# Kernel tuning notes

Hardware: AMD Instinct MI355X
Metric: run time of the kernel (lower is better)

The kernel has to match this reference:

```python
import jax, jax.numpy as jnp
import numpy as np

N, E, T, H, D_IN, D_OUT = 50000, 320000, 4, 4, 128, 128
NEG_SLOPE = 0.2
LN_EPS = 1e-5


def setup_inputs() -> dict:
    key = jax.random.key(0)
    ks = jax.random.split(key, 10)
    x = jax.random.normal(ks[0], (N, D_IN), jnp.float32)
    edge_index = jax.random.randint(ks[1], (2, E), 0, N, jnp.int32)
    edge_attr = jax.random.randint(ks[2], (E,), 0, T, jnp.int32)
    W_gat = jax.random.normal(ks[3], (T, D_IN, H * D_OUT), jnp.float32) / np.sqrt(D_IN)
    a_src = jax.random.normal(ks[4], (T, H, D_OUT), jnp.float32) / np.sqrt(D_OUT)
    a_dst = jax.random.normal(ks[5], (T, H, D_OUT), jnp.float32) / np.sqrt(D_OUT)
    b_gat = jnp.zeros((T, D_OUT), jnp.float32)
    edge_type_weights = jnp.ones((T,), jnp.float32) / T
    W_fuse = jax.random.normal(ks[6], (T * D_OUT, D_OUT), jnp.float32) / np.sqrt(T * D_OUT)
    b_fuse = jnp.zeros((D_OUT,), jnp.float32)
    ln_gamma = jnp.ones((D_OUT,), jnp.float32)
    ln_beta = jnp.zeros((D_OUT,), jnp.float32)
    return {"x": x, "edge_index": edge_index, "edge_attr": edge_attr,
            "W_gat": W_gat, "a_src": a_src, "a_dst": a_dst, "b_gat": b_gat,
            "edge_type_weights": edge_type_weights, "W_fuse": W_fuse,
            "b_fuse": b_fuse, "ln_gamma": ln_gamma, "ln_beta": ln_beta}


def _gat_one_type(x, src_all, dst_all, mask_all, W, a_s, a_d, b):
    # x: [N, D_in]; src_all/dst_all: [E+N] (type-mask + self-loops on all nodes)
    n = x.shape[0]
    h = (x @ W).reshape(n, H, D_OUT)                      # [N, H, D]
    alpha_s = jnp.sum(h * a_s, axis=-1)                   # [N, H]
    alpha_d = jnp.sum(h * a_d, axis=-1)                   # [N, H]
    logit = jax.nn.leaky_relu(alpha_s[src_all] + alpha_d[dst_all], NEG_SLOPE)  # [Ea, H]
    neg_inf = jnp.float32(-1e30)
    logit = jnp.where(mask_all[:, None], logit, neg_inf)
    m = jax.ops.segment_max(logit, dst_all, num_segments=n)   # [N, H] (self-loops ensure finite)
    ex = jnp.exp(logit - m[dst_all])
    ex = jnp.where(mask_all[:, None], ex, 0.0)
    denom = jax.ops.segment_sum(ex, dst_all, num_segments=n)  # [N, H]
    alpha = ex / denom[dst_all]                                # [Ea, H]
    msg = alpha[:, :, None] * h[src_all]                       # [Ea, H, D]
    out = jax.ops.segment_sum(msg, dst_all, num_segments=n)   # [N, H, D]
    return out.mean(axis=1) + b                                # concat=False -> head mean


def reference(x, edge_index, edge_attr, W_gat, a_src, a_dst, b_gat,
              edge_type_weights, W_fuse, b_fuse, ln_gamma, ln_beta):
    n = x.shape[0]
    self_idx = jnp.arange(n, dtype=edge_index.dtype)
    src_all = jnp.concatenate([edge_index[0], self_idx])
    dst_all = jnp.concatenate([edge_index[1], self_idx])
    outs = []
    for t in range(T):
        mask_all = jnp.concatenate([edge_attr == t, jnp.ones((n,), bool)])
        outs.append(_gat_one_type(x, src_all, dst_all, mask_all,
                                  W_gat[t], a_src[t], a_dst[t], b_gat[t]))
    w = jax.nn.softmax(edge_type_weights)
    x_cat = jnp.concatenate([outs[t] * w[t] for t in range(T)], axis=1)  # [N, T*D]
    y = x_cat @ W_fuse + b_fuse
    mu = jnp.mean(y, axis=-1, keepdims=True)
    var = jnp.var(y, axis=-1, keepdims=True)
    y = (y - mu) / jnp.sqrt(var + LN_EPS) * ln_gamma + ln_beta
    return jax.nn.relu(y)
```

## Files before the change

kernel.cpp:

```cpp
#include <hip/hip_runtime.h>
#include <hip/hip_bf16.h>

#define TT 4
#define HH 4
#define DD 128
#define KAGG 2048

typedef __attribute__((ext_vector_type(8))) short short8;
typedef __attribute__((ext_vector_type(4))) float f32x4;
typedef __attribute__((ext_vector_type(4))) unsigned int uint4v;

__device__ __forceinline__ float lrelu(float z) { return z > 0.f ? z : 0.2f * z; }
__device__ __forceinline__ float bf2f(unsigned short u) {
  union { unsigned int i; float f; } v; v.i = ((unsigned int)u) << 16; return v.f;
}
__device__ __forceinline__ unsigned short f2b(float f) {
  union { float f; unsigned int i; } u; u.f = f;
  unsigned int r = u.i + 0x7fff + ((u.i >> 16) & 1);
  return (unsigned short)(r >> 16);
}
__device__ __forceinline__ void unpack8v(uint4v u, float* hv) {
  hv[0] = bf2f((unsigned short)(u.x & 0xffff));
  hv[1] = bf2f((unsigned short)(u.x >> 16));
  hv[2] = bf2f((unsigned short)(u.y & 0xffff));
  hv[3] = bf2f((unsigned short)(u.y >> 16));
  hv[4] = bf2f((unsigned short)(u.z & 0xffff));
  hv[5] = bf2f((unsigned short)(u.z >> 16));
  hv[6] = bf2f((unsigned short)(u.w & 0xffff));
  hv[7] = bf2f((unsigned short)(u.w >> 16));
}

__global__ __launch_bounds__(256) void prologue_kernel(
    const float* __restrict__ x, unsigned short* __restrict__ xb, int total4,
    const float* __restrict__ Wg, const float* __restrict__ a_s,
    const float* __restrict__ a_d, const float* __restrict__ W_fuse,
    const float* __restrict__ b_gat, const float* __restrict__ etw,
    const float* __restrict__ b_fuse, unsigned short* __restrict__ Pall,
    float* __restrict__ cbias, const int* __restrict__ dst,
    const int* __restrict__ attr, int* __restrict__ deg, int E, int N) {
  int bid = blockIdx.x;
  const int nconv = (total4 + 255) >> 8;
  if (bid < nconv) {
    int i = bid * 256 + threadIdx.x;
    if (i < total4) {
      float4 v = ((const float4*)x)[i];
      ushort4 o;
      o.x = f2b(v.x); o.y = f2b(v.y); o.z = f2b(v.z); o.w = f2b(v.w);
      ((ushort4*)xb)[i] = o;
    }
    return;
  }
  bid -= nconv;
  if (bid < 17) {
    float e0 = etw[0], e1 = etw[1], e2 = etw[2], e3 = etw[3];
    float mx = fmaxf(fmaxf(e0, e1), fmaxf(e2, e3));
    float w0 = __expf(e0 - mx), w1 = __expf(e1 - mx), w2 = __expf(e2 - mx),
          w3 = __expf(e3 - mx);
    float inv = 1.f / (w0 + w1 + w2 + w3);
    float wts[4] = {w0 * inv, w1 * inv, w2 * inv, w3 * inv};
    if (bid < 16) {
      int idx = bid * 256 + threadIdx.x;
      int c = idx >> 7, k = idx & 127;
      int t = c >> 3, jj = c & 7, head = jj & 3;
      const float* av = ((jj < 4) ? a_s : a_d) + (t * 4 + head) * 128;
      const float* wr = Wg + (size_t)t * 65536 + k * 512 + head * 128;
      float s = 0.f;
      for (int m = 0; m < 128; ++m) s += wr[m] * av[m];
      Pall[c * 128 + k] = f2b(s);
    } else {
      int j = threadIdx.x;
      if (j < 128) {
        float s = b_fuse[j];
        for (int t = 0; t < 4; ++t) {
          float st = 0.f;
          for (int m = 0; m < 128; ++m)
            st += b_gat[t * 128 + m] * W_fuse[(size_t)(t * 128 + m) * 128 + j];
          s += wts[t] * st;
        }
        cbias[j] = s;
      }
    }
    return;
  }
  bid -= 17;
  int e = bid * 256 + threadIdx.x;
  if (e < E) atomicAdd(&deg[attr[e] * N + dst[e]], 1);
}

__global__ __launch_bounds__(256) void gprep_kernel(
    const float* __restrict__ Wg, const float* __restrict__ W_fuse,
    const float* __restrict__ etw, unsigned short* __restrict__ Gfrag) {
  __shared__ float Bs[128][128];
  int t = blockIdx.x >> 6;
  int kr0 = (blockIdx.x & 63) * 8;
  const float* wf = W_fuse + (size_t)t * 16384;
#pragma unroll
  for (int i = 0; i < 64; ++i)
    ((float*)Bs)[i * 256 + threadIdx.x] = wf[i * 256 + threadIdx.x];

  float e0 = etw[0], e1 = etw[1], e2 = etw[2], e3 = etw[3];
  float mx = fmaxf(fmaxf(e0, e1), fmaxf(e2, e3));
  float w0 = __expf(e0 - mx), w1 = __expf(e1 - mx), w2 = __expf(e2 - mx),
        w3 = __expf(e3 - mx);
  float inv = 1.f / (w0 + w1 + w2 + w3);
  float wt = ((t == 0) ? w0 : (t == 1) ? w1 : (t == 2) ? w2 : w3) * inv * 0.25f;
  __syncthreads();

  int rr = threadIdx.x >> 7;
  int j  = threadIdx.x & 127;
#pragma unroll
  for (int r2 = 0; r2 < 4; ++r2) {
    int kr = kr0 + r2 * 2 + rr;
    int head = kr >> 7, k = kr & 127;
    const float* wr = Wg + (size_t)t * 65536 + k * 512 + head * 128;
    float s = 0.f;
    for (int m = 0; m < 128; ++m) s += wr[m] * Bs[m][j];
    s *= wt;
    int K = t * 512 + kr;
    int kt = K >> 7, kk = (K >> 5) & 3, n = j >> 4;
    int f = (kt * 4 + kk) * 8 + n;
    int lg = (K >> 3) & 3, lr = j & 15, j8 = K & 7;
    Gfrag[(size_t)f * 512 + (lg * 16 + lr) * 8 + j8] = f2b(s);
  }
}

__global__ __launch_bounds__(1024) void scanfused_kernel(
    const int* __restrict__ deg, int* __restrict__ rowptr,
    int* __restrict__ cursor, int* __restrict__ gcur, int M) {
  __shared__ int sh[1024];
  __shared__ int base;
  int i = blockIdx.x * 1024 + threadIdx.x;
  int v = (i < M) ? deg[i] : 0;
  sh[threadIdx.x] = v;
  __syncthreads();
  for (int off = 1; off < 1024; off <<= 1) {
    int xx = (threadIdx.x >= off) ? sh[threadIdx.x - off] : 0;
    __syncthreads();
    sh[threadIdx.x] += xx;
    __syncthreads();
  }
  if (threadIdx.x == 1023) base = atomicAdd(gcur, sh[1023]);
  __syncthreads();
  if (i < M) {
    int r = base + sh[threadIdx.x] - v;
    rowptr[i] = r;
    cursor[i] = r;
  }
}

__global__ __launch_bounds__(256) void scatter_alpha_kernel(
    const int* __restrict__ src, const int* __restrict__ dst,
    const int* __restrict__ attr, int* __restrict__ cursor,
    int* __restrict__ slist, const unsigned short* __restrict__ xb,
    const unsigned short* __restrict__ Pall, float* __restrict__ as_,
    float* __restrict__ ad_, int E, int N) {
  __shared__ uint4 ldsv[2048];
  int bid = blockIdx.x;
  const int nsc = (E + 255) >> 8;
  if (bid < nsc) {
    int e = bid * 256 + threadIdx.x;
    if (e < E) {
      int p = atomicAdd(&cursor[attr[e] * N + dst[e]], 1);
      slist[p] = src[e];
    }
    return;
  }
  bid -= nsc;
  unsigned char* lds = (unsigned char*)ldsv;
  const int n0 = bid * 128;
  const int tid = threadIdx.x, lane = tid & 63, wid = tid >> 6;
  const int lr = lane & 15, lg = lane >> 4;
#pragma unroll
  for (int i = 0; i < 8; ++i) {
    int chunk = tid + i * 256;
    int row = chunk >> 4, k16 = chunk & 15;
    int gr = n0 + row;
    uint4 v = make_uint4(0, 0, 0, 0);
    if (gr < N) v = *(const uint4*)(xb + (size_t)gr * DD + k16 * 8);
    *(uint4*)(lds + ((row * 256 + k16 * 16) ^ ((row & 7) << 4))) = v;
  }
  __syncthreads();
  f32x4 acc[2][2] = {};
#pragma unroll
  for (int kk = 0; kk < 4; ++kk) {
    short8 a[2], b[2];
#pragma unroll
    for (int m = 0; m < 2; ++m) {
      int row = wid * 32 + m * 16 + lr;
      a[m] = *(const short8*)(lds + ((row * 256 + kk * 64 + (lg << 4)) ^ ((row & 7) << 4)));
    }
#pragma unroll
    for (int n = 0; n < 2; ++n) {
      int c = n * 16 + lr;
      b[n] = *(const short8*)(Pall + c * DD + kk * 32 + lg * 8);
    }
#pragma unroll
    for (int m = 0; m < 2; ++m)
#pragma unroll
      for (int n = 0; n < 2; ++n)
        acc[m][n] = __builtin_amdgcn_mfma_f32_16x16x32_bf16(a[m], b[n], acc[m][n], 0, 0, 0);
  }
#pragma unroll
  for (int m = 0; m < 2; ++m)
#pragma unroll
    for (int n = 0; n < 2; ++n) {
      int c = n * 16 + lr;
      int t = c >> 3, jj = c & 7, head = jj & 3;
      float* dstp = (jj & 4) ? ad_ : as_;
#pragma unroll
      for (int r = 0; r < 4; ++r) {
        int gr = n0 + wid * 32 + m * 16 + lg * 4 + r;
        if (gr < N) dstp[((size_t)t * N + gr) * 4 + head] = acc[m][n][r];
      }
    }
}

__global__ __launch_bounds__(256) void gather_kernel(
    const int* __restrict__ slist, const int* __restrict__ rowptr,
    const int* __restrict__ deg, const float* __restrict__ as_,
    const float* __restrict__ ad_, const unsigned short* __restrict__ xb,
    unsigned short* __restrict__ AGG, int N) {
  int t = blockIdx.y;
  int lane = threadIdx.x & 63;
  int u = lane >> 4, c16 = lane & 15;
  int d = blockIdx.x * 16 + (threadIdx.x >> 6) * 4 + u;
  if (d >= N) return;
  size_t tn = (size_t)t * N;
  int dofs = c16 * 8;
  unsigned short* outp = AGG + (size_t)d * KAGG + t * 512 + dofs;

  int base = rowptr[tn + d], dg = deg[tn + d];
  uint4v uself = *(const uint4v*)(xb + (size_t)d * DD + dofs);
  if (dg == 0) {
#pragma unroll
    for (int h = 0; h < 4; ++h) *(uint4v*)(outp + h * DD) = uself;
    return;
  }

  float4 ad4 = *(const float4*)(ad_ + (tn + d) * 4);
  float4 av = *(const float4*)(as_ + (tn + d) * 4);
  float q[4], den[4], hv[8], acc[4][8];
  q[0] = __expf(lrelu(av.x + ad4.x));
  q[1] = __expf(lrelu(av.y + ad4.y));
  q[2] = __expf(lrelu(av.z + ad4.z));
  q[3] = __expf(lrelu(av.w + ad4.w));
  unpack8v(uself, hv);
#pragma unroll
  for (int h = 0; h < 4; ++h) {
    den[h] = q[h];
#pragma unroll
    for (int j = 0; j < 8; ++j) acc[h][j] = q[h] * hv[j];
  }

  int i = 0;
  for (; i + 3 < dg; i += 4) {
    int s0 = slist[base + i], s1 = slist[base + i + 1];
    int s2 = slist[base + i + 2], s3 = slist[base + i + 3];
    float4 a0 = *(const float4*)(as_ + (tn + s0) * 4);
    float4 a1 = *(const float4*)(as_ + (tn + s1) * 4);
    float4 a2 = *(const float4*)(as_ + (tn + s2) * 4);
    float4 a3 = *(const float4*)(as_ + (tn + s3) * 4);
    uint4v u0 = *(const uint4v*)(xb + (size_t)s0 * DD + dofs);
    uint4v u1 = *(const uint4v*)(xb + (size_t)s1 * DD + dofs);
    uint4v u2 = *(const uint4v*)(xb + (size_t)s2 * DD + dofs);
    uint4v u3 = *(const uint4v*)(xb + (size_t)s3 * DD + dofs);
    float qq[4][4];
    qq[0][0] = __expf(lrelu(a0.x + ad4.x));
    qq[0][1] = __expf(lrelu(a0.y + ad4.y));
    qq[0][2] = __expf(lrelu(a0.z + ad4.z));
    qq[0][3] = __expf(lrelu(a0.w + ad4.w));
    qq[1][0] = __expf(lrelu(a1.x + ad4.x));
    qq[1][1] = __expf(lrelu(a1.y + ad4.y));
    qq[1][2] = __expf(lrelu(a1.z + ad4.z));
    qq[1][3] = __expf(lrelu(a1.w + ad4.w));
    qq[2][0] = __expf(lrelu(a2.x + ad4.x));
    qq[2][1] = __expf(lrelu(a2.y + ad4.y));
    qq[2][2] = __expf(lrelu(a2.z + ad4.z));
    qq[2][3] = __expf(lrelu(a2.w + ad4.w));
    qq[3][0] = __expf(lrelu(a3.x + ad4.x));
    qq[3][1] = __expf(lrelu(a3.y + ad4.y));
    qq[3][2] = __expf(lrelu(a3.z + ad4.z));
    qq[3][3] = __expf(lrelu(a3.w + ad4.w));
#pragma unroll
    for (int h = 0; h < 4; ++h)
      den[h] += qq[0][h] + qq[1][h] + qq[2][h] + qq[3][h];
    unpack8v(u0, hv);
#pragma unroll
    for (int h = 0; h < 4; ++h)
#pragma unroll
      for (int j = 0; j < 8; ++j) acc[h][j] += qq[0][h] * hv[j];
    unpack8v(u1, hv);
#pragma unroll
    for (int h = 0; h < 4; ++h)
#pragma unroll
      for (int j = 0; j < 8; ++j) acc[h][j] += qq[1][h] * hv[j];
    unpack8v(u2, hv);
#pragma unroll
    for (int h = 0; h < 4; ++h)
#pragma unroll
      for (int j = 0; j < 8; ++j) acc[h][j] += qq[2][h] * hv[j];
    unpack8v(u3, hv);
#pragma unroll
    for (int h = 0; h < 4; ++h)
#pragma unroll
      for (int j = 0; j < 8; ++j) acc[h][j] += qq[3][h] * hv[j];
  }
  for (; i < dg; ++i) {
    int s = slist[base + i];
    float4 a = *(const float4*)(as_ + (tn + s) * 4);
    uint4v ue = *(const uint4v*)(xb + (size_t)s * DD + dofs);
    float qe[4];
    qe[0] = __expf(lrelu(a.x + ad4.x));
    qe[1] = __expf(lrelu(a.y + ad4.y));
    qe[2] = __expf(lrelu(a.z + ad4.z));
    qe[3] = __expf(lrelu(a.w + ad4.w));
#pragma unroll
    for (int h = 0; h < 4; ++h) den[h] += qe[h];
    unpack8v(ue, hv);
#pragma unroll
    for (int h = 0; h < 4; ++h)
#pragma unroll
      for (int j = 0; j < 8; ++j) acc[h][j] += qe[h] * hv[j];
  }

#pragma unroll
  for (int h = 0; h < 4; ++h) {
    float r = 1.f / den[h];
    uint4v o;
    o.x = (unsigned)f2b(acc[h][0] * r) | ((unsigned)f2b(acc[h][1] * r) << 16);
    o.y = (unsigned)f2b(acc[h][2] * r) | ((unsigned)f2b(acc[h][3] * r) << 16);
    o.z = (unsigned)f2b(acc[h][4] * r) | ((unsigned)f2b(acc[h][5] * r) << 16);
    o.w = (unsigned)f2b(acc[h][6] * r) | ((unsigned)f2b(acc[h][7] * r) << 16);
    *(uint4v*)(outp + h * DD) = o;
  }
}

__global__ __launch_bounds__(256) void gemmln_kernel(
    const unsigned short* __restrict__ AGG, const unsigned short* __restrict__ Gfrag,
    const float* __restrict__ cbias, const float* __restrict__ gamma,
    const float* __restrict__ beta, float* __restrict__ out, int N) {
  __shared__ uint4 bbuf[2][1024];
  const int n0 = blockIdx.x * 64;
  const int tid = threadIdx.x, lane = tid & 63, wid = tid >> 6;
  const int lr = lane & 15, lg = lane >> 4;
  const int wrow = n0 + wid * 16;
  const int gr = wrow + lr;
  const bool ok = gr < N;
  const unsigned short* arow = AGG + (size_t)gr * KAGG;

  uint4 bn[4], an[2], ac[2];
#pragma unroll
  for (int i = 0; i < 4; ++i)
    bn[i] = *(const uint4*)(Gfrag + (size_t)(i * 256 + tid) * 8);
#pragma unroll
  for (int kkh = 0; kkh < 2; ++kkh) {
    an[kkh] = make_uint4(0, 0, 0, 0);
    if (ok) an[kkh] = *(const uint4*)(arow + kkh * 32 + lg * 8);
  }
#pragma unroll
  for (int i = 0; i < 4; ++i) bbuf[0][i * 256 + tid] = bn[i];
  ac[0] = an[0]; ac[1] = an[1];
  __syncthreads();

  f32x4 acc[8] = {};
  int cur = 0;
  for (int ht = 0; ht < 32; ++ht) {
    if (ht < 31) {
#pragma unroll
      for (int i = 0; i < 4; ++i)
        bn[i] = *(const uint4*)(Gfrag + (size_t)(ht + 1) * 8192 +
                                (size_t)(i * 256 + tid) * 8);
#pragma unroll
      for (int kkh = 0; kkh < 2; ++kkh) {
        an[kkh] = make_uint4(0, 0, 0, 0);
        if (ok) an[kkh] = *(const uint4*)(arow + (ht + 1) * 64 + kkh * 32 + lg * 8);
      }
    }
    const unsigned char* lds = (const unsigned char*)bbuf[cur];
#pragma unroll
    for (int kkh = 0; kkh < 2; ++kkh) {
      short8 a = *(const short8*)&ac[kkh];
#pragma unroll
      for (int n = 0; n < 8; ++n) {
        short8 b = *(const short8*)(lds + (kkh * 8 + n) * 1024 + lane * 16);
        acc[n] = __builtin_amdgcn_mfma_f32_16x16x32_bf16(a, b, acc[n], 0, 0, 0);
      }
    }
    if (ht < 31) {
#pragma unroll
      for (int i = 0; i < 4; ++i) bbuf[cur ^ 1][i * 256 + tid] = bn[i];
      ac[0] = an[0]; ac[1] = an[1];
      __syncthreads();
      cur ^= 1;
    }
  }

  float cb[8], gm[8], bt[8];
#pragma unroll
  for (int n = 0; n < 8; ++n) {
    cb[n] = cbias[n * 16 + lr];
    gm[n] = gamma[n * 16 + lr];
    bt[n] = beta[n * 16 + lr];
  }
#pragma unroll
  for (int rr = 0; rr < 4; ++rr) {
    float y[8];
    float s = 0.f, ss = 0.f;
#pragma unroll
    for (int n = 0; n < 8; ++n) {
      y[n] = acc[n][rr] + cb[n];
      s += y[n];
      ss += y[n] * y[n];
    }
#pragma unroll
    for (int mask = 1; mask <= 8; mask <<= 1) {
      s += __shfl_xor(s, mask);
      ss += __shfl_xor(ss, mask);
    }
    float mean = s * (1.f / 128.f);
    float var = ss * (1.f / 128.f) - mean * mean;
    float rstd = rsqrtf(var + 1e-5f);
    int orow = wrow + lg * 4 + rr;
    if (orow < N) {
#pragma unroll
      for (int n = 0; n < 8; ++n) {
        float v = (y[n] - mean) * rstd * gm[n] + bt[n];
        out[(size_t)orow * DD + n * 16 + lr] = fmaxf(0.f, v);
      }
    }
  }
}

extern "C" void kernel_launch(void* const* d_in, const int* in_sizes, int n_in,
                              void* d_out, int out_size, void* d_ws, size_t ws_size,
                              hipStream_t stream) {
  const float* x      = (const float*)d_in[0];
  const int*   ei     = (const int*)d_in[1];
  const int*   attr   = (const int*)d_in[2];
  const float* Wg     = (const float*)d_in[3];
  const float* a_src  = (const float*)d_in[4];
  const float* a_dst  = (const float*)d_in[5];
  const float* b_gat  = (const float*)d_in[6];
  const float* etw    = (const float*)d_in[7];
  const float* W_fuse = (const float*)d_in[8];
  const float* b_fuse = (const float*)d_in[9];
  const float* gamma  = (const float*)d_in[10];
  const float* beta   = (const float*)d_in[11];

  const int N = in_sizes[0] / DD;
  const int E = in_sizes[2];
  const int* src = ei;
  const int* dst = ei + E;
  const int M = TT * N;

  char* ws = (char*)d_ws;
  size_t off = 0;
  auto alloc = [&](size_t bytes) {
    void* p = ws + off;
    off += (bytes + 255) & ~(size_t)255;
    return p;
  };
  unsigned short* AGG   = (unsigned short*)alloc((size_t)N * KAGG * 2);
  unsigned short* xb    = (unsigned short*)alloc((size_t)N * DD * 2);
  unsigned short* Gfrag = (unsigned short*)alloc((size_t)512 * 512 * 2);
  unsigned short* Pall  = (unsigned short*)alloc((size_t)32 * DD * 2);
  float* cbias          = (float*)alloc(128 * sizeof(float));
  float* as_            = (float*)alloc((size_t)TT * N * 4 * sizeof(float));
  float* ad_            = (float*)alloc((size_t)TT * N * 4 * sizeof(float));
  int* deg              = (int*)alloc((size_t)(M + 1) * sizeof(int));
  int* rowptr           = (int*)alloc((size_t)M * sizeof(int));
  int* cursor           = (int*)alloc((size_t)M * sizeof(int));
  int* slist            = (int*)alloc((size_t)E * sizeof(int));

  hipMemsetAsync(deg, 0, (size_t)(M + 1) * sizeof(int), stream);

  int total4x = N * DD / 4;
  int nconv = (total4x + 255) / 256;
  int nhist = (E + 255) / 256;
  prologue_kernel<<<nconv + 17 + nhist, 256, 0, stream>>>(
      x, xb, total4x, Wg, a_src, a_dst, W_fuse, b_gat, etw, b_fuse,
      Pall, cbias, dst, attr, deg, E, N);

  gprep_kernel<<<256, 256, 0, stream>>>(Wg, W_fuse, etw, Gfrag);

  scanfused_kernel<<<(M + 1023) / 1024, 1024, 0, stream>>>(deg, rowptr, cursor,
                                                           deg + M, M);

  int nalpha = (N + 127) / 128;
  scatter_alpha_kernel<<<nhist + nalpha, 256, 0, stream>>>(
      src, dst, attr, cursor, slist, xb, Pall, as_, ad_, E, N);

  dim3 ggrid((N + 15) / 16, TT);
  gather_kernel<<<ggrid, 256, 0, stream>>>(slist, rowptr, deg, as_, ad_, xb, AGG, N);

  gemmln_kernel<<<(N + 63) / 64, 256, 0, stream>>>(AGG, Gfrag, cbias, gamma, beta,
                                                   (float*)d_out, N);
}
```

Measured before the change: 210.5 us.

## Merge scan, weight prep and alpha GEMM into one launch; precompute edge exp weights

The scan, fused-weight preparation and per-node alpha projection now run as block-index-partitioned branches of a single stage2 kernel with a shared 64KB LDS buffer, which cuts launches. The edge scatter moves into its own kernel that also computes each edge's exp(leaky_relu) attention numerators and stores them in a new qlist beside the CSR source list. The gather kernel then streams these precomputed weights instead of gathering as_ per source and evaluating exp, and its unroll drops from 4 to 2. In exchange there is an extra 16 bytes per edge of writes and reads, a dependent kernel boundary between alpha computation and scatter, and scan blocks that now hold 64KB of LDS, which may lower occupancy.

```diff
diff --git a/kernel.cpp b/kernel.cpp
--- a/kernel.cpp
+++ b/kernel.cpp
@@ -87,86 +87,76 @@
   if (e < E) atomicAdd(&deg[attr[e] * N + dst[e]], 1);
 }
 
-__global__ __launch_bounds__(256) void gprep_kernel(
+__global__ __launch_bounds__(256) void stage2_kernel(
+    const int* __restrict__ deg, int* __restrict__ rowptr,
+    int* __restrict__ cursor, int* __restrict__ gcur, int M,
     const float* __restrict__ Wg, const float* __restrict__ W_fuse,
-    const float* __restrict__ etw, unsigned short* __restrict__ Gfrag) {
-  __shared__ float Bs[128][128];
-  int t = blockIdx.x >> 6;
-  int kr0 = (blockIdx.x & 63) * 8;
-  const float* wf = W_fuse + (size_t)t * 16384;
-#pragma unroll
-  for (int i = 0; i < 64; ++i)
-    ((float*)Bs)[i * 256 + threadIdx.x] = wf[i * 256 + threadIdx.x];
-
-  float e0 = etw[0], e1 = etw[1], e2 = etw[2], e3 = etw[3];
-  float mx = fmaxf(fmaxf(e0, e1), fmaxf(e2, e3));
-  float w0 = __expf(e0 - mx), w1 = __expf(e1 - mx), w2 = __expf(e2 - mx),
-        w3 = __expf(e3 - mx);
-  float inv = 1.f / (w0 + w1 + w2 + w3);
-  float wt = ((t == 0) ? w0 : (t == 1) ? w1 : (t == 2) ? w2 : w3) * inv * 0.25f;
-  __syncthreads();
-
-  int rr = threadIdx.x >> 7;
-  int j  = threadIdx.x & 127;
-#pragma unroll
-  for (int r2 = 0; r2 < 4; ++r2) {
-    int kr = kr0 + r2 * 2 + rr;
-    int head = kr >> 7, k = kr & 127;
-    const float* wr = Wg + (size_t)t * 65536 + k * 512 + head * 128;
-    float s = 0.f;
-    for (int m = 0; m < 128; ++m) s += wr[m] * Bs[m][j];
-    s *= wt;
-    int K = t * 512 + kr;
-    int kt = K >> 7, kk = (K >> 5) & 3, n = j >> 4;
-    int f = (kt * 4 + kk) * 8 + n;
-    int lg = (K >> 3) & 3, lr = j & 15, j8 = K & 7;
-    Gfrag[(size_t)f * 512 + (lg * 16 + lr) * 8 + j8] = f2b(s);
-  }
-}
-
-__global__ __launch_bounds__(1024) void scanfused_kernel(
-    const int* __restrict__ deg, int* __restrict__ rowptr,
-    int* __restrict__ cursor, int* __restrict__ gcur, int M) {
-  __shared__ int sh[1024];
-  __shared__ int base;
-  int i = blockIdx.x * 1024 + threadIdx.x;
-  int v = (i < M) ? deg[i] : 0;
-  sh[threadIdx.x] = v;
-  __syncthreads();
-  for (int off = 1; off < 1024; off <<= 1) {
-    int xx = (threadIdx.x >= off) ? sh[threadIdx.x - off] : 0;
+    const float* __restrict__ etw, unsigned short* __restrict__ Gfrag,
+    const unsigned short* __restrict__ xb, const unsigned short* __restrict__ Pall,
+    float* __restrict__ as_, float* __restrict__ ad_, int N) {
+  __shared__ __align__(16) unsigned char smem[65536 + 16];
+  int bid = blockIdx.x;
+  const int nscan = (M + 255) >> 8;
+  if (bid < nscan) {
+    int* sh = (int*)smem;
+    int* basep = (int*)(smem + 65536);
+    int i = bid * 256 + threadIdx.x;
+    int v = (i < M) ? deg[i] : 0;
+    sh[threadIdx.x] = v;
     __syncthreads();
-    sh[threadIdx.x] += xx;
+    for (int off = 1; off < 256; off <<= 1) {
+      int xx = (threadIdx.x >= off) ? sh[threadIdx.x - off] : 0;
+      __syncthreads();
+      sh[threadIdx.x] += xx;
+      __syncthreads();
+    }
+    if (threadIdx.x == 255) *basep = atomicAdd(gcur, sh[255]);
     __syncthreads();
-  }
-  if (threadIdx.x == 1023) base = atomicAdd(gcur, sh[1023]);
-  __syncthreads();
-  if (i < M) {
-    int r = base + sh[threadIdx.x] - v;
-    rowptr[i] = r;
-    cursor[i] = r;
-  }
-}
-
-__global__ __launch_bounds__(256) void scatter_alpha_kernel(
-    const int* __restrict__ src, const int* __restrict__ dst,
-    const int* __restrict__ attr, int* __restrict__ cursor,
-    int* __restrict__ slist, const unsigned short* __restrict__ xb,
-    const unsigned short* __restrict__ Pall, float* __restrict__ as_,
-    float* __restrict__ ad_, int E, int N) {
-  __shared__ uint4 ldsv[2048];
-  int bid = blockIdx.x;
-  const int nsc = (E + 255) >> 8;
-  if (bid < nsc) {
-    int e = bid * 256 + threadIdx.x;
-    if (e < E) {
-      int p = atomicAdd(&cursor[attr[e] * N + dst[e]], 1);
-      slist[p] = src[e];
+    if (i < M) {
+      int r = *basep + sh[threadIdx.x] - v;
+      rowptr[i] = r;
+      cursor[i] = r;
     }
     return;
   }
-  bid -= nsc;
-  unsigned char* lds = (unsigned char*)ldsv;
+  bid -= nscan;
+  if (bid < 256) {
+    float(*Bs)[128] = (float(*)[128])smem;
+    int t = bid >> 6;
+    int kr0 = (bid & 63) * 8;
+    const float* wf = W_fuse + (size_t)t * 16384;
+#pragma unroll
+    for (int i = 0; i < 64; ++i)
+      ((float*)Bs)[i * 256 + threadIdx.x] = wf[i * 256 + threadIdx.x];
+
+    float e0 = etw[0], e1 = etw[1], e2 = etw[2], e3 = etw[3];
+    float mx = fmaxf(fmaxf(e0, e1), fmaxf(e2, e3));
+    float w0 = __expf(e0 - mx), w1 = __expf(e1 - mx), w2 = __expf(e2 - mx),
+          w3 = __expf(e3 - mx);
+    float inv = 1.f / (w0 + w1 + w2 + w3);
+    float wt = ((t == 0) ? w0 : (t == 1) ? w1 : (t == 2) ? w2 : w3) * inv * 0.25f;
+    __syncthreads();
+
+    int rr = threadIdx.x >> 7;
+    int j = threadIdx.x & 127;
+#pragma unroll
+    for (int r2 = 0; r2 < 4; ++r2) {
+      int kr = kr0 + r2 * 2 + rr;
+      int head = kr >> 7, k = kr & 127;
+      const float* wr = Wg + (size_t)t * 65536 + k * 512 + head * 128;
+      float s = 0.f;
+      for (int m = 0; m < 128; ++m) s += wr[m] * Bs[m][j];
+      s *= wt;
+      int K = t * 512 + kr;
+      int kt = K >> 7, kk = (K >> 5) & 3, n = j >> 4;
+      int f = (kt * 4 + kk) * 8 + n;
+      int lg = (K >> 3) & 3, lr = j & 15, j8 = K & 7;
+      Gfrag[(size_t)f * 512 + (lg * 16 + lr) * 8 + j8] = f2b(s);
+    }
+    return;
+  }
+  bid -= 256;
+  unsigned char* lds = smem;
   const int n0 = bid * 128;
   const int tid = threadIdx.x, lane = tid & 63, wid = tid >> 6;
   const int lr = lane & 15, lg = lane >> 4;
@@ -215,11 +205,33 @@
     }
 }
 
+__global__ __launch_bounds__(256) void scatter_q_kernel(
+    const int* __restrict__ src, const int* __restrict__ dst,
+    const int* __restrict__ attr, int* __restrict__ cursor,
+    int* __restrict__ slist, float* __restrict__ qlist,
+    const float* __restrict__ as_, const float* __restrict__ ad_,
+    int E, int N) {
+  int e = blockIdx.x * 256 + threadIdx.x;
+  if (e >= E) return;
+  int t = attr[e], s = src[e], d = dst[e];
+  int p = atomicAdd(&cursor[(size_t)t * N + d], 1);
+  float4 a = *(const float4*)(as_ + ((size_t)t * N + s) * 4);
+  float4 b = *(const float4*)(ad_ + ((size_t)t * N + d) * 4);
+  float4 q;
+  q.x = __expf(lrelu(a.x + b.x));
+  q.y = __expf(lrelu(a.y + b.y));
+  q.z = __expf(lrelu(a.z + b.z));
+  q.w = __expf(lrelu(a.w + b.w));
+  slist[p] = s;
+  *(float4*)(qlist + (size_t)p * 4) = q;
+}
+
 __global__ __launch_bounds__(256) void gather_kernel(
-    const int* __restrict__ slist, const int* __restrict__ rowptr,
-    const int* __restrict__ deg, const float* __restrict__ as_,
-    const float* __restrict__ ad_, const unsigned short* __restrict__ xb,
-    unsigned short* __restrict__ AGG, int N) {
+    const int* __restrict__ slist, const float* __restrict__ qlist,
+    const int* __restrict__ rowptr, const int* __restrict__ deg,
+    const float* __restrict__ as_, const float* __restrict__ ad_,
+    const unsigned short* __restrict__ xb, unsigned short* __restrict__ AGG,
+    int N) {
   int t = blockIdx.y;
   int lane = threadIdx.x & 63;
   int u = lane >> 4, c16 = lane & 15;
@@ -239,81 +251,49 @@
 
   float4 ad4 = *(const float4*)(ad_ + (tn + d) * 4);
   float4 av = *(const float4*)(as_ + (tn + d) * 4);
-  float q[4], den[4], hv[8], acc[4][8];
-  q[0] = __expf(lrelu(av.x + ad4.x));
-  q[1] = __expf(lrelu(av.y + ad4.y));
-  q[2] = __expf(lrelu(av.z + ad4.z));
-  q[3] = __expf(lrelu(av.w + ad4.w));
-  unpack8v(uself, hv);
-#pragma unroll
-  for (int h = 0; h < 4; ++h) {
-    den[h] = q[h];
-#pragma unroll
-    for (int j = 0; j < 8; ++j) acc[h][j] = q[h] * hv[j];
+  float den[4], hv[8], acc[4][8];
+  {
+    float qs[4];
+    qs[0] = __expf(lrelu(av.x + ad4.x));
+    qs[1] = __expf(lrelu(av.y + ad4.y));
+    qs[2] = __expf(lrelu(av.z + ad4.z));
+    qs[3] = __expf(lrelu(av.w + ad4.w));
+    unpack8v(uself, hv);
+#pragma unroll
+    for (int h = 0; h < 4; ++h) {
+      den[h] = qs[h];
+#pragma unroll
+      for (int j = 0; j < 8; ++j) acc[h][j] = qs[h] * hv[j];
+    }
   }
 
   int i = 0;
-  for (; i + 3 < dg; i += 4) {
+  for (; i + 1 < dg; i += 2) {
     int s0 = slist[base + i], s1 = slist[base + i + 1];
-    int s2 = slist[base + i + 2], s3 = slist[base + i + 3];
-    float4 a0 = *(const float4*)(as_ + (tn + s0) * 4);
-    float4 a1 = *(const float4*)(as_ + (tn + s1) * 4);
-    float4 a2 = *(const float4*)(as_ + (tn + s2) * 4);
-    float4 a3 = *(const float4*)(as_ + (tn + s3) * 4);
+    float4 q0 = *(const float4*)(qlist + (size_t)(base + i) * 4);
+    float4 q1 = *(const float4*)(qlist + (size_t)(base + i + 1) * 4);
     uint4v u0 = *(const uint4v*)(xb + (size_t)s0 * DD + dofs);
     uint4v u1 = *(const uint4v*)(xb + (size_t)s1 * DD + dofs);
-    uint4v u2 = *(const uint4v*)(xb + (size_t)s2 * DD + dofs);
-    uint4v u3 = *(const uint4v*)(xb + (size_t)s3 * DD + dofs);
-    float qq[4][4];
-    qq[0][0] = __expf(lrelu(a0.x + ad4.x));
-    qq[0][1] = __expf(lrelu(a0.y + ad4.y));
-    qq[0][2] = __expf(lrelu(a0.z + ad4.z));
-    qq[0][3] = __expf(lrelu(a0.w + ad4.w));
-    qq[1][0] = __expf(lrelu(a1.x + ad4.x));
-    qq[1][1] = __expf(lrelu(a1.y + ad4.y));
-    qq[1][2] = __expf(lrelu(a1.z + ad4.z));
-    qq[1][3] = __expf(lrelu(a1.w + ad4.w));
-    qq[2][0] = __expf(lrelu(a2.x + ad4.x));
-    qq[2][1] = __expf(lrelu(a2.y + ad4.y));
-    qq[2][2] = __expf(lrelu(a2.z + ad4.z));
-    qq[2][3] = __expf(lrelu(a2.w + ad4.w));
-    qq[3][0] = __expf(lrelu(a3.x + ad4.x));
-    qq[3][1] = __expf(lrelu(a3.y + ad4.y));
-    qq[3][2] = __expf(lrelu(a3.z + ad4.z));
-    qq[3][3] = __expf(lrelu(a3.w + ad4.w));
+    float qa[4] = {q0.x, q0.y, q0.z, q0.w};
+    float qb[4] = {q1.x, q1.y, q1.z, q1.w};
+#pragma unroll
+    for (int h = 0; h < 4; ++h) den[h] += qa[h] + qb[h];
+    unpack8v(u0, hv);
 #pragma unroll
     for (int h = 0; h < 4; ++h)
-      den[h] += qq[0][h] + qq[1][h] + qq[2][h] + qq[3][h];
-    unpack8v(u0, hv);
+#pragma unroll
+      for (int j = 0; j < 8; ++j) acc[h][j] += qa[h] * hv[j];
+    unpack8v(u1, hv);
 #pragma unroll
     for (int h = 0; h < 4; ++h)
 #pragma unroll
-      for (int j = 0; j < 8; ++j) acc[h][j] += qq[0][h] * hv[j];
-    unpack8v(u1, hv);
-#pragma unroll
-    for (int h = 0; h < 4; ++h)
-#pragma unroll
-      for (int j = 0; j < 8; ++j) acc[h][j] += qq[1][h] * hv[j];
-    unpack8v(u2, hv);
-#pragma unroll
-    for (int h = 0; h < 4; ++h)
-#pragma unroll
-      for (int j = 0; j < 8; ++j) acc[h][j] += qq[2][h] * hv[j];
-    unpack8v(u3, hv);
-#pragma unroll
-    for (int h = 0; h < 4; ++h)
-#pragma unroll
-      for (int j = 0; j < 8; ++j) acc[h][j] += qq[3][h] * hv[j];
-  }
-  for (; i < dg; ++i) {
+      for (int j = 0; j < 8; ++j) acc[h][j] += qb[h] * hv[j];
+  }
+  if (i < dg) {
     int s = slist[base + i];
-    float4 a = *(const float4*)(as_ + (tn + s) * 4);
+    float4 q = *(const float4*)(qlist + (size_t)(base + i) * 4);
     uint4v ue = *(const uint4v*)(xb + (size_t)s * DD + dofs);
-    float qe[4];
-    qe[0] = __expf(lrelu(a.x + ad4.x));
-    qe[1] = __expf(lrelu(a.y + ad4.y));
-    qe[2] = __expf(lrelu(a.z + ad4.z));
-    qe[3] = __expf(lrelu(a.w + ad4.w));
+    float qe[4] = {q.x, q.y, q.z, q.w};
 #pragma unroll
     for (int h = 0; h < 4; ++h) den[h] += qe[h];
     unpack8v(ue, hv);
@@ -471,6 +451,7 @@
   int* rowptr           = (int*)alloc((size_t)M * sizeof(int));
   int* cursor           = (int*)alloc((size_t)M * sizeof(int));
   int* slist            = (int*)alloc((size_t)E * sizeof(int));
+  float* qlist          = (float*)alloc((size_t)E * 4 * sizeof(float));
 
   hipMemsetAsync(deg, 0, (size_t)(M + 1) * sizeof(int), stream);
 
@@ -481,17 +462,18 @@
       x, xb, total4x, Wg, a_src, a_dst, W_fuse, b_gat, etw, b_fuse,
       Pall, cbias, dst, attr, deg, E, N);
 
-  gprep_kernel<<<256, 256, 0, stream>>>(Wg, W_fuse, etw, Gfrag);
-
-  scanfused_kernel<<<(M + 1023) / 1024, 1024, 0, stream>>>(deg, rowptr, cursor,
-                                                           deg + M, M);
-
+  int nscan = (M + 255) / 256;
   int nalpha = (N + 127) / 128;
-  scatter_alpha_kernel<<<nhist + nalpha, 256, 0, stream>>>(
-      src, dst, attr, cursor, slist, xb, Pall, as_, ad_, E, N);
+  stage2_kernel<<<nscan + 256 + nalpha, 256, 0, stream>>>(
+      deg, rowptr, cursor, deg + M, M, Wg, W_fuse, etw, Gfrag,
+      xb, Pall, as_, ad_, N);
+
+  scatter_q_kernel<<<nhist, 256, 0, stream>>>(src, dst, attr, cursor, slist,
+                                              qlist, as_, ad_, E, N);
 
   dim3 ggrid((N + 15) / 16, TT);
-  gather_kernel<<<ggrid, 256, 0, stream>>>(slist, rowptr, deg, as_, ad_, xb, AGG, N);
+  gather_kernel<<<ggrid, 256, 0, stream>>>(slist, qlist, rowptr, deg, as_, ad_,
+                                           xb, AGG, N);
 
   gemmln_kernel<<<(N + 63) / 64, 256, 0, stream>>>(AGG, Gfrag, cbias, gamma, beta,
                                                    (float*)d_out, N);
```

Result: no change. 211.5 us (+0.5%).

## Split GEMM-LN output columns across 8 waves and shrink gather unroll

Applied to the files above, without the earlier changes.

The fused GEMM+LayerNorm kernel now runs 512 threads per block: two groups of four waves each compute half of the 128 output columns for the same 64 rows. Per-row LayerNorm partial sums are exchanged through shared memory with an extra barrier. This is meant to halve per-wave accumulators and raise occupancy and latency hiding, but each wave in the block loads the same A rows again. Separately, the gather loop unroll drops from 4 to 2 edges, reducing register pressure but also the number of memory loads in flight.

```diff
diff --git a/kernel.cpp b/kernel.cpp
--- a/kernel.cpp
+++ b/kernel.cpp
@@ -253,59 +253,35 @@
   }
 
   int i = 0;
-  for (; i + 3 < dg; i += 4) {
+  for (; i + 1 < dg; i += 2) {
     int s0 = slist[base + i], s1 = slist[base + i + 1];
-    int s2 = slist[base + i + 2], s3 = slist[base + i + 3];
     float4 a0 = *(const float4*)(as_ + (tn + s0) * 4);
     float4 a1 = *(const float4*)(as_ + (tn + s1) * 4);
-    float4 a2 = *(const float4*)(as_ + (tn + s2) * 4);
-    float4 a3 = *(const float4*)(as_ + (tn + s3) * 4);
     uint4v u0 = *(const uint4v*)(xb + (size_t)s0 * DD + dofs);
     uint4v u1 = *(const uint4v*)(xb + (size_t)s1 * DD + dofs);
-    uint4v u2 = *(const uint4v*)(xb + (size_t)s2 * DD + dofs);
-    uint4v u3 = *(const uint4v*)(xb + (size_t)s3 * DD + dofs);
-    float qq[4][4];
-    qq[0][0] = __expf(lrelu(a0.x + ad4.x));
-    qq[0][1] = __expf(lrelu(a0.y + ad4.y));
-    qq[0][2] = __expf(lrelu(a0.z + ad4.z));
-    qq[0][3] = __expf(lrelu(a0.w + ad4.w));
-    qq[1][0] = __expf(lrelu(a1.x + ad4.x));
-    qq[1][1] = __expf(lrelu(a1.y + ad4.y));
-    qq[1][2] = __expf(lrelu(a1.z + ad4.z));
-    qq[1][3] = __expf(lrelu(a1.w + ad4.w));
-    qq[2][0] = __expf(lrelu(a2.x + ad4.x));
-    qq[2][1] = __expf(lrelu(a2.y + ad4.y));
-    qq[2][2] = __expf(lrelu(a2.z + ad4.z));
-    qq[2][3] = __expf(lrelu(a2.w + ad4.w));
-    qq[3][0] = __expf(lrelu(a3.x + ad4.x));
-    qq[3][1] = __expf(lrelu(a3.y + ad4.y));
-    qq[3][2] = __expf(lrelu(a3.z + ad4.z));
-    qq[3][3] = __expf(lrelu(a3.w + ad4.w));
+    float q0[4], q1[4];
+    q0[0] = __expf(lrelu(a0.x + ad4.x));
+    q0[1] = __expf(lrelu(a0.y + ad4.y));
+    q0[2] = __expf(lrelu(a0.z + ad4.z));
+    q0[3] = __expf(lrelu(a0.w + ad4.w));
+    q1[0] = __expf(lrelu(a1.x + ad4.x));
+    q1[1] = __expf(lrelu(a1.y + ad4.y));
+    q1[2] = __expf(lrelu(a1.z + ad4.z));
+    q1[3] = __expf(lrelu(a1.w + ad4.w));
+#pragma unroll
+    for (int h = 0; h < 4; ++h) den[h] += q0[h] + q1[h];
+    unpack8v(u0, hv);
 #pragma unroll
     for (int h = 0; h < 4; ++h)
-      den[h] += qq[0][h] + qq[1][h] + qq[2][h] + qq[3][h];
-    unpack8v(u0, hv);
+#pragma unroll
+      for (int j = 0; j < 8; ++j) acc[h][j] += q0[h] * hv[j];
+    unpack8v(u1, hv);
 #pragma unroll
     for (int h = 0; h < 4; ++h)
 #pragma unroll
-      for (int j = 0; j < 8; ++j) acc[h][j] += qq[0][h] * hv[j];
-    unpack8v(u1, hv);
-#pragma unroll
-    for (int h = 0; h < 4; ++h)
-#pragma unroll
-      for (int j = 0; j < 8; ++j) acc[h][j] += qq[1][h] * hv[j];
-    unpack8v(u2, hv);
-#pragma unroll
-    for (int h = 0; h < 4; ++h)
-#pragma unroll
-      for (int j = 0; j < 8; ++j) acc[h][j] += qq[2][h] * hv[j];
-    unpack8v(u3, hv);
-#pragma unroll
-    for (int h = 0; h < 4; ++h)
-#pragma unroll
-      for (int j = 0; j < 8; ++j) acc[h][j] += qq[3][h] * hv[j];
-  }
-  for (; i < dg; ++i) {
+      for (int j = 0; j < 8; ++j) acc[h][j] += q1[h] * hv[j];
+  }
+  if (i < dg) {
     int s = slist[base + i];
     float4 a = *(const float4*)(as_ + (tn + s) * 4);
     uint4v ue = *(const uint4v*)(xb + (size_t)s * DD + dofs);
@@ -335,41 +311,42 @@
   }
 }
 
-__global__ __launch_bounds__(256) void gemmln_kernel(
+__global__ __launch_bounds__(512) void gemmln_kernel(
     const unsigned short* __restrict__ AGG, const unsigned short* __restrict__ Gfrag,
     const float* __restrict__ cbias, const float* __restrict__ gamma,
     const float* __restrict__ beta, float* __restrict__ out, int N) {
   __shared__ uint4 bbuf[2][1024];
-  const int n0 = blockIdx.x * 64;
+  __shared__ float lnbuf[256];
   const int tid = threadIdx.x, lane = tid & 63, wid = tid >> 6;
   const int lr = lane & 15, lg = lane >> 4;
-  const int wrow = n0 + wid * 16;
-  const int gr = wrow + lr;
+  const int rw = wid & 3, cw = wid >> 2;
+  const int n0 = blockIdx.x * 64;
+  const int gr = n0 + rw * 16 + lr;
   const bool ok = gr < N;
   const unsigned short* arow = AGG + (size_t)gr * KAGG;
 
-  uint4 bn[4], an[2], ac[2];
-#pragma unroll
-  for (int i = 0; i < 4; ++i)
-    bn[i] = *(const uint4*)(Gfrag + (size_t)(i * 256 + tid) * 8);
+  uint4 bn[2], an[2], ac[2];
+#pragma unroll
+  for (int i = 0; i < 2; ++i)
+    bn[i] = *(const uint4*)(Gfrag + (size_t)(i * 512 + tid) * 8);
 #pragma unroll
   for (int kkh = 0; kkh < 2; ++kkh) {
     an[kkh] = make_uint4(0, 0, 0, 0);
     if (ok) an[kkh] = *(const uint4*)(arow + kkh * 32 + lg * 8);
   }
 #pragma unroll
-  for (int i = 0; i < 4; ++i) bbuf[0][i * 256 + tid] = bn[i];
+  for (int i = 0; i < 2; ++i) bbuf[0][i * 512 + tid] = bn[i];
   ac[0] = an[0]; ac[1] = an[1];
   __syncthreads();
 
-  f32x4 acc[8] = {};
+  f32x4 acc[4] = {};
   int cur = 0;
   for (int ht = 0; ht < 32; ++ht) {
     if (ht < 31) {
 #pragma unroll
-      for (int i = 0; i < 4; ++i)
+      for (int i = 0; i < 2; ++i)
         bn[i] = *(const uint4*)(Gfrag + (size_t)(ht + 1) * 8192 +
-                                (size_t)(i * 256 + tid) * 8);
+                                (size_t)(i * 512 + tid) * 8);
 #pragma unroll
       for (int kkh = 0; kkh < 2; ++kkh) {
         an[kkh] = make_uint4(0, 0, 0, 0);
@@ -381,51 +358,62 @@
     for (int kkh = 0; kkh < 2; ++kkh) {
       short8 a = *(const short8*)&ac[kkh];
 #pragma unroll
-      for (int n = 0; n < 8; ++n) {
-        short8 b = *(const short8*)(lds + (kkh * 8 + n) * 1024 + lane * 16);
+      for (int n = 0; n < 4; ++n) {
+        short8 b = *(const short8*)(lds + (kkh * 8 + cw * 4 + n) * 1024 + lane * 16);
         acc[n] = __builtin_amdgcn_mfma_f32_16x16x32_bf16(a, b, acc[n], 0, 0, 0);
       }
     }
     if (ht < 31) {
 #pragma unroll
-      for (int i = 0; i < 4; ++i) bbuf[cur ^ 1][i * 256 + tid] = bn[i];
+      for (int i = 0; i < 2; ++i) bbuf[cur ^ 1][i * 512 + tid] = bn[i];
       ac[0] = an[0]; ac[1] = an[1];
       __syncthreads();
       cur ^= 1;
     }
   }
 
-  float cb[8], gm[8], bt[8];
-#pragma unroll
-  for (int n = 0; n < 8; ++n) {
-    cb[n] = cbias[n * 16 + lr];
-    gm[n] = gamma[n * 16 + lr];
-    bt[n] = beta[n * 16 + lr];
+  float cb[4], gm[4], bt[4];
+#pragma unroll
+  for (int n = 0; n < 4; ++n) {
+    int col = cw * 64 + n * 16 + lr;
+    cb[n] = cbias[col];
+    gm[n] = gamma[col];
+    bt[n] = beta[col];
   }
 #pragma unroll
   for (int rr = 0; rr < 4; ++rr) {
-    float y[8];
     float s = 0.f, ss = 0.f;
 #pragma unroll
-    for (int n = 0; n < 8; ++n) {
-      y[n] = acc[n][rr] + cb[n];
-      s += y[n];
-      ss += y[n] * y[n];
-    }
-#pragma unroll
-    for (int mask = 1; mask <= 8; mask <<= 1) {
-      s += __shfl_xor(s, mask);
-      ss += __shfl_xor(ss, mask);
-    }
-    float mean = s * (1.f / 128.f);
-    float var = ss * (1.f / 128.f) - mean * mean;
-    float rstd = rsqrtf(var + 1e-5f);
-    int orow = wrow + lg * 4 + rr;
+    for (int n = 0; n < 4; ++n) {
+      float y = acc[n][rr] + cb[n];
+      s += y;
+      ss += y * y;
+    }
+    s += __shfl_xor(s, 1); ss += __shfl_xor(ss, 1);
+    s += __shfl_xor(s, 2); ss += __shfl_xor(ss, 2);
+    s += __shfl_xor(s, 4); ss += __shfl_xor(ss, 4);
+    s += __shfl_xor(s, 8); ss += __shfl_xor(ss, 8);
+    if (lr == 0) {
+      int row64 = rw * 16 + lg * 4 + rr;
+      lnbuf[cw * 64 + row64] = s;
+      lnbuf[128 + cw * 64 + row64] = ss;
+    }
+  }
+  __syncthreads();
+#pragma unroll
+  for (int rr = 0; rr < 4; ++rr) {
+    int row64 = rw * 16 + lg * 4 + rr;
+    int orow = n0 + row64;
     if (orow < N) {
-#pragma unroll
-      for (int n = 0; n < 8; ++n) {
-        float v = (y[n] - mean) * rstd * gm[n] + bt[n];
-        out[(size_t)orow * DD + n * 16 + lr] = fmaxf(0.f, v);
+      float st = lnbuf[row64] + lnbuf[64 + row64];
+      float sst = lnbuf[128 + row64] + lnbuf[192 + row64];
+      float mean = st * (1.f / 128.f);
+      float var = sst * (1.f / 128.f) - mean * mean;
+      float rstd = rsqrtf(var + 1e-5f);
+#pragma unroll
+      for (int n = 0; n < 4; ++n) {
+        float v = (acc[n][rr] + cb[n] - mean) * rstd * gm[n] + bt[n];
+        out[(size_t)orow * DD + cw * 64 + n * 16 + lr] = fmaxf(0.f, v);
       }
     }
   }
@@ -493,6 +481,6 @@
   dim3 ggrid((N + 15) / 16, TT);
   gather_kernel<<<ggrid, 256, 0, stream>>>(slist, rowptr, deg, as_, ad_, xb, AGG, N);
 
-  gemmln_kernel<<<(N + 63) / 64, 256, 0, stream>>>(AGG, Gfrag, cbias, gamma, beta,
+  gemmln_kernel<<<(N + 63) / 64, 512, 0, stream>>>(AGG, Gfrag, cbias, gamma, beta,
                                                    (float*)d_out, N);
 }
```

Result: slower. 230.3 us (+9.4%).
